# Performance work log

Measured on AMD Instinct MI355X. Metric: run time of the kernel, lower is better.

Reference implementation:

```python
import jax, jax.numpy as jnp
import numpy as np

N, M, K, C, OUT = 200000, 50000, 16, 64, 128
EPS = 1e-5  # torch BatchNorm1d default eps


def _bn(h, gamma, beta, mean, var):
    # BatchNorm1d in eval mode (running statistics)
    return (h - mean) * jax.lax.rsqrt(var + EPS) * gamma + beta


def setup_inputs() -> dict:
    key = jax.random.key(0)
    ks = jax.random.split(key, 8)
    p = jax.random.normal(ks[0], (N, 3), jnp.float32)
    x = jax.random.normal(ks[1], (N, C), jnp.float32)
    idx = jax.random.randint(ks[2], (M,), 0, N)          # FPS-sampled center indices
    knn_idx = jax.random.randint(ks[3], (M, K), 0, N)    # KNN neighbor indices
    # channel_shrinker: Linear(3+C, C, bias=False) -> BN -> ReLU -> Linear(C, 1)
    W1 = jax.random.normal(ks[4], (3 + C, C), jnp.float32) * 0.05  # stored [in,out]
    g1 = jnp.ones((C,), jnp.float32); b1 = jnp.zeros((C,), jnp.float32)
    m1 = jnp.zeros((C,), jnp.float32); v1 = jnp.ones((C,), jnp.float32)
    W2 = jax.random.normal(ks[5], (C, 1), jnp.float32) * 0.05
    b2 = jnp.zeros((1,), jnp.float32)
    # linear2: Linear(C, OUT, bias=False) -> BN -> ReLU
    Wl = jax.random.normal(ks[6], (C, OUT), jnp.float32) * 0.05
    gl = jnp.ones((OUT,), jnp.float32); bl = jnp.zeros((OUT,), jnp.float32)
    ml = jnp.zeros((OUT,), jnp.float32); vl = jnp.ones((OUT,), jnp.float32)
    return {"p": p, "x": x, "W1": W1, "g1": g1, "b1": b1, "m1": m1, "v1": v1,
            "W2": W2, "b2": b2, "Wl": Wl, "gl": gl, "bl": bl, "ml": ml, "vl": vl,
            "idx": idx, "knn_idx": knn_idx}


def reference(p, x, W1, g1, b1, m1, v1, W2, b2, Wl, gl, bl, ml, vl, idx, knn_idx):
    # queryandgroup(use_xyz=True): relative xyz of neighbors + gathered features
    n_p = p[idx]                                   # [M,3] sampled centers
    rel = p[knn_idx] - n_p[:, None, :]             # [M,K,3]
    x_knn = jnp.concatenate([rel, x[knn_idx]], -1) # [M,K,3+C]
    # channel_shrinker
    h = jnp.maximum(_bn(x_knn @ W1, g1, b1, m1, v1), 0.0)   # [M,K,C]
    s = h @ W2 + b2                                          # [M,K,1]
    prob = jax.nn.softmax(s, axis=1)                         # softmax over neighbors
    # linear2 on ALL original points, then gather by knn_idx
    y = jnp.maximum(_bn(x @ Wl, gl, bl, ml, vl), 0.0)        # [N,OUT]
    y_knn = y[knn_idx]                                       # [M,K,OUT]
    out = jnp.sum(y_knn * prob, axis=1)                      # [M,OUT]
    return n_p, out
```

## Files before the change

### kernel.cpp

```cpp
#include <hip/hip_runtime.h>

#define EPS 1e-5f

typedef __attribute__((ext_vector_type(8))) short bf16x8;
typedef __attribute__((ext_vector_type(4))) float f32x4;

static __device__ __forceinline__ unsigned short f2bf(float f) {
  unsigned int u = __float_as_uint(f);
  u = u + 0x7FFFu + ((u >> 16) & 1u);
  return (unsigned short)(u >> 16);
}
static __device__ __forceinline__ float bf2f(unsigned short h) {
  return __uint_as_float(((unsigned int)h) << 16);
}
static __device__ __forceinline__ unsigned int pk2(float lo, float hi) {
  return (unsigned int)f2bf(lo) | ((unsigned int)f2bf(hi) << 16);
}

__global__ __launch_bounds__(256) void k1_mfma(
    const float* __restrict__ x, const float* __restrict__ W1,
    const float* __restrict__ Wl, const float* __restrict__ gl,
    const float* __restrict__ bl, const float* __restrict__ ml,
    const float* __restrict__ vl,
    unsigned short* __restrict__ Z, unsigned short* __restrict__ Y)
{
  __shared__ unsigned short As[64 * 64];
  __shared__ unsigned short Bs[192 * 64];
  char* Ab = reinterpret_cast<char*>(As);
  char* Bb = reinterpret_cast<char*>(Bs);

  const int t = threadIdx.x;
  const long row0 = (long)blockIdx.x * 64;

  {
    int k = t >> 2, c0 = (t & 3) * 16;
    const float4* w4 = reinterpret_cast<const float4*>(W1 + (size_t)(3 + k) * 64 + c0);
#pragma unroll
    for (int i = 0; i < 4; ++i) {
      float4 w = w4[i];
#pragma unroll
      for (int j = 0; j < 4; ++j) {
        int c = c0 + i * 4 + j;
        float v = (j == 0) ? w.x : (j == 1) ? w.y : (j == 2) ? w.z : w.w;
        int byte = c * 128 + ((2 * k) ^ ((c & 7) << 4));
        *reinterpret_cast<unsigned short*>(Bb + byte) = f2bf(v);
      }
    }
  }
  {
    int k = t >> 2, c0 = (t & 3) * 32;
    const float4* w4 = reinterpret_cast<const float4*>(Wl + (size_t)k * 128 + c0);
#pragma unroll
    for (int i = 0; i < 8; ++i) {
      float4 w = w4[i];
#pragma unroll
      for (int j = 0; j < 4; ++j) {
        int c = 64 + c0 + i * 4 + j;
        float v = (j == 0) ? w.x : (j == 1) ? w.y : (j == 2) ? w.z : w.w;
        int byte = c * 128 + ((2 * k) ^ ((c & 7) << 4));
        *reinterpret_cast<unsigned short*>(Bb + byte) = f2bf(v);
      }
    }
  }
  {
    const float4* xg = reinterpret_cast<const float4*>(x + row0 * 64);
#pragma unroll
    for (int i = 0; i < 4; ++i) {
      int idx = t + i * 256;
      float4 v = xg[idx];
      int r = idx >> 4;
      int b0 = (idx & 15) * 8;
      int byte = r * 128 + (b0 ^ ((r & 7) << 4));
      uint2 pk = make_uint2(pk2(v.x, v.y), pk2(v.z, v.w));
      *reinterpret_cast<uint2*>(Ab + byte) = pk;
    }
  }
  __syncthreads();

  const int wid = t >> 6, lane = t & 63;
  const int roff = (wid & 1) * 32, coff = (wid >> 1) * 96;
  const int lr = lane & 15, lk = lane >> 4;

  bf16x8 af[2][2];
#pragma unroll
  for (int rt = 0; rt < 2; ++rt) {
    int r = roff + rt * 16 + lr;
#pragma unroll
    for (int ks = 0; ks < 2; ++ks) {
      int byte = r * 128 + ((ks * 64 + lk * 16) ^ ((r & 7) << 4));
      af[rt][ks] = *reinterpret_cast<const bf16x8*>(Ab + byte);
    }
  }

#pragma unroll
  for (int ct = 0; ct < 6; ++ct) {
    int c = coff + ct * 16 + lr;
    int byte0 = c * 128 + ((lk * 16) ^ ((c & 7) << 4));
    int byte1 = c * 128 + ((64 + lk * 16) ^ ((c & 7) << 4));
    bf16x8 bf0 = *reinterpret_cast<const bf16x8*>(Bb + byte0);
    bf16x8 bf1 = *reinterpret_cast<const bf16x8*>(Bb + byte1);

    float sc = 1.f, sh = 0.f;
    if (c >= 64) {
      int oc = c - 64;
      sc = gl[oc] * rsqrtf(vl[oc] + EPS);
      sh = bl[oc] - ml[oc] * sc;
    }
#pragma unroll
    for (int rt = 0; rt < 2; ++rt) {
      f32x4 acc = {0.f, 0.f, 0.f, 0.f};
      acc = __builtin_amdgcn_mfma_f32_16x16x32_bf16(af[rt][0], bf0, acc, 0, 0, 0);
      acc = __builtin_amdgcn_mfma_f32_16x16x32_bf16(af[rt][1], bf1, acc, 0, 0, 0);
      long grow = row0 + roff + rt * 16 + lk * 4;
      if (c < 64) {
#pragma unroll
        for (int q = 0; q < 4; ++q)
          Z[(grow + q) * 64 + c] = f2bf(acc[q]);
      } else {
        int oc = c - 64;
#pragma unroll
        for (int q = 0; q < 4; ++q) {
          float yv = fmaxf(fmaf(acc[q], sc, sh), 0.f);
          Y[(grow + q) * 128 + oc] = f2bf(yv);
        }
      }
    }
  }
}

__global__ __launch_bounds__(256) void k2_gather(
    const float* __restrict__ p, const unsigned short* __restrict__ Z,
    const unsigned short* __restrict__ Y, const float* __restrict__ W1,
    const float* __restrict__ g1, const float* __restrict__ b1,
    const float* __restrict__ m1, const float* __restrict__ v1,
    const float* __restrict__ W2, const int* __restrict__ idx,
    const int* __restrict__ knn, float* __restrict__ out_np,
    float* __restrict__ out_feat, int M)
{
  int gtid = blockIdx.x * 256 + threadIdx.x;
  int wid = gtid >> 6;
  int lane = threadIdx.x & 63;
  if (wid >= M) return;
  int m = __builtin_amdgcn_readfirstlane(wid);

  float a1 = g1[lane] * rsqrtf(v1[lane] + EPS);
  float c1 = b1[lane] - m1[lane] * a1;
  float w2 = W2[lane];
  float w10 = W1[lane];
  float w11 = W1[64 + lane];
  float w12 = W1[128 + lane];

  int ic = idx[m];
  float cx = p[ic * 3 + 0];
  float cy = p[ic * 3 + 1];
  float cz = p[ic * 3 + 2];
  if (lane < 3) {
    float v = (lane == 0) ? cx : ((lane == 1) ? cy : cz);
    out_np[(size_t)m * 3 + lane] = v;
  }

  float s[16];
  int jj[16];
#pragma unroll
  for (int k = 0; k < 16; ++k) {
    int j = knn[m * 16 + k];
    jj[k] = j;
    float rx = p[j * 3 + 0] - cx;
    float ry = p[j * 3 + 1] - cy;
    float rz = p[j * 3 + 2] - cz;
    float tv = bf2f(Z[(size_t)j * 64 + lane]);
    tv = fmaf(rx, w10, tv);
    tv = fmaf(ry, w11, tv);
    tv = fmaf(rz, w12, tv);
    float h = fmaxf(fmaf(tv, a1, c1), 0.f);
    float part = h * w2;
#pragma unroll
    for (int off = 32; off > 0; off >>= 1)
      part += __shfl_xor(part, off, 64);
    s[k] = part;
  }

  float mx = s[0];
#pragma unroll
  for (int k = 1; k < 16; ++k) mx = fmaxf(mx, s[k]);
  float sum = 0.f;
#pragma unroll
  for (int k = 0; k < 16; ++k) { s[k] = __expf(s[k] - mx); sum += s[k]; }
  float inv = 1.f / sum;

  float acc0 = 0.f, acc1 = 0.f;
#pragma unroll
  for (int k = 0; k < 16; ++k) {
    const unsigned short* yr = Y + (size_t)jj[k] * 128;
    unsigned int u = *reinterpret_cast<const unsigned int*>(yr + 2 * lane);
    acc0 = fmaf(s[k], bf2f((unsigned short)(u & 0xFFFFu)), acc0);
    acc1 = fmaf(s[k], bf2f((unsigned short)(u >> 16)), acc1);
  }
  float* orow = out_feat + (size_t)m * 128;
  *reinterpret_cast<float2*>(orow + 2 * lane) =
      make_float2(acc0 * inv, acc1 * inv);
}

extern "C" void kernel_launch(void* const* d_in, const int* in_sizes, int n_in,
                              void* d_out, int out_size, void* d_ws, size_t ws_size,
                              hipStream_t stream) {
  const float* p  = (const float*)d_in[0];
  const float* x  = (const float*)d_in[1];
  const float* W1 = (const float*)d_in[2];
  const float* g1 = (const float*)d_in[3];
  const float* b1 = (const float*)d_in[4];
  const float* m1 = (const float*)d_in[5];
  const float* v1 = (const float*)d_in[6];
  const float* W2 = (const float*)d_in[7];
  const float* Wl = (const float*)d_in[9];
  const float* gl = (const float*)d_in[10];
  const float* bl = (const float*)d_in[11];
  const float* ml = (const float*)d_in[12];
  const float* vl = (const float*)d_in[13];
  const int* idx  = (const int*)d_in[14];
  const int* knn  = (const int*)d_in[15];

  const int N = in_sizes[1] / 64;
  const int M = in_sizes[14];

  unsigned short* Z = (unsigned short*)d_ws;
  unsigned short* Y = Z + (size_t)N * 64;
  float* out_np   = (float*)d_out;
  float* out_feat = out_np + (size_t)M * 3;

  k1_mfma<<<dim3(N / 64), dim3(256), 0, stream>>>(
      x, W1, Wl, gl, bl, ml, vl, Z, Y);
  k2_gather<<<dim3(((size_t)M * 64 + 255) / 256), dim3(256), 0, stream>>>(
      p, Z, Y, W1, g1, b1, m1, v1, W2, idx, knn, out_np, out_feat, M);
}
```

Baseline: 219.7 us.

## Vectorize k1 output stores via swapped MFMA operands and batch k2 shuffle reductions

```diff
diff --git a/kernel.cpp b/kernel.cpp
--- a/kernel.cpp
+++ b/kernel.cpp
@@ -71,8 +71,8 @@
       int r = idx >> 4;
       int b0 = (idx & 15) * 8;
       int byte = r * 128 + (b0 ^ ((r & 7) << 4));
-      uint2 pk = make_uint2(pk2(v.x, v.y), pk2(v.z, v.w));
-      *reinterpret_cast<uint2*>(Ab + byte) = pk;
+      uint2 pkv = make_uint2(pk2(v.x, v.y), pk2(v.z, v.w));
+      *reinterpret_cast<uint2*>(Ab + byte) = pkv;
     }
   }
   __syncthreads();
@@ -94,38 +94,54 @@
 
 #pragma unroll
   for (int ct = 0; ct < 6; ++ct) {
-    int c = coff + ct * 16 + lr;
-    int byte0 = c * 128 + ((lk * 16) ^ ((c & 7) << 4));
-    int byte1 = c * 128 + ((64 + lk * 16) ^ ((c & 7) << 4));
+    int c0t = coff + ct * 16;
+    int cread = c0t + lr;
+    int byte0 = cread * 128 + ((lk * 16) ^ ((cread & 7) << 4));
+    int byte1 = cread * 128 + ((64 + lk * 16) ^ ((cread & 7) << 4));
     bf16x8 bf0 = *reinterpret_cast<const bf16x8*>(Bb + byte0);
     bf16x8 bf1 = *reinterpret_cast<const bf16x8*>(Bb + byte1);
 
-    float sc = 1.f, sh = 0.f;
-    if (c >= 64) {
-      int oc = c - 64;
-      sc = gl[oc] * rsqrtf(vl[oc] + EPS);
-      sh = bl[oc] - ml[oc] * sc;
+    float sc0 = 1.f, sc1 = 1.f, sc2 = 1.f, sc3 = 1.f;
+    float sh0 = 0.f, sh1 = 0.f, sh2 = 0.f, sh3 = 0.f;
+    if (c0t >= 64) {
+      int oc = c0t - 64 + lk * 4;
+      float4 g4 = *reinterpret_cast<const float4*>(gl + oc);
+      float4 v4 = *reinterpret_cast<const float4*>(vl + oc);
+      float4 b4 = *reinterpret_cast<const float4*>(bl + oc);
+      float4 m4 = *reinterpret_cast<const float4*>(ml + oc);
+      sc0 = g4.x * rsqrtf(v4.x + EPS); sh0 = b4.x - m4.x * sc0;
+      sc1 = g4.y * rsqrtf(v4.y + EPS); sh1 = b4.y - m4.y * sc1;
+      sc2 = g4.z * rsqrtf(v4.z + EPS); sh2 = b4.z - m4.z * sc2;
+      sc3 = g4.w * rsqrtf(v4.w + EPS); sh3 = b4.w - m4.w * sc3;
     }
 #pragma unroll
     for (int rt = 0; rt < 2; ++rt) {
       f32x4 acc = {0.f, 0.f, 0.f, 0.f};
-      acc = __builtin_amdgcn_mfma_f32_16x16x32_bf16(af[rt][0], bf0, acc, 0, 0, 0);
-      acc = __builtin_amdgcn_mfma_f32_16x16x32_bf16(af[rt][1], bf1, acc, 0, 0, 0);
-      long grow = row0 + roff + rt * 16 + lk * 4;
-      if (c < 64) {
-#pragma unroll
-        for (int q = 0; q < 4; ++q)
-          Z[(grow + q) * 64 + c] = f2bf(acc[q]);
+      acc = __builtin_amdgcn_mfma_f32_16x16x32_bf16(bf0, af[rt][0], acc, 0, 0, 0);
+      acc = __builtin_amdgcn_mfma_f32_16x16x32_bf16(bf1, af[rt][1], acc, 0, 0, 0);
+      long n = row0 + roff + rt * 16 + lr;
+      if (c0t < 64) {
+        int cb = c0t + lk * 4;
+        *reinterpret_cast<ushort4*>(Z + n * 64 + cb) =
+            make_ushort4(f2bf(acc[0]), f2bf(acc[1]), f2bf(acc[2]), f2bf(acc[3]));
       } else {
-        int oc = c - 64;
-#pragma unroll
-        for (int q = 0; q < 4; ++q) {
-          float yv = fmaxf(fmaf(acc[q], sc, sh), 0.f);
-          Y[(grow + q) * 128 + oc] = f2bf(yv);
-        }
+        int cb = c0t - 64 + lk * 4;
+        float y0 = fmaxf(fmaf(acc[0], sc0, sh0), 0.f);
+        float y1 = fmaxf(fmaf(acc[1], sc1, sh1), 0.f);
+        float y2 = fmaxf(fmaf(acc[2], sc2, sh2), 0.f);
+        float y3 = fmaxf(fmaf(acc[3], sc3, sh3), 0.f);
+        *reinterpret_cast<ushort4*>(Y + n * 128 + cb) =
+            make_ushort4(f2bf(y0), f2bf(y1), f2bf(y2), f2bf(y3));
       }
     }
   }
+}
+
+static __device__ __forceinline__ float comb(float a, float b, int off, int lane) {
+  bool hi = (lane & off) != 0;
+  float send = hi ? a : b;
+  float t = __shfl_xor(send, off, 64);
+  return (hi ? b : a) + t;
 }
 
 __global__ __launch_bounds__(256) void k2_gather(
@@ -159,7 +175,7 @@
     out_np[(size_t)m * 3 + lane] = v;
   }
 
-  float s[16];
+  float part[16];
   int jj[16];
 #pragma unroll
   for (int k = 0; k < 16; ++k) {
@@ -173,28 +189,46 @@
     tv = fmaf(ry, w11, tv);
     tv = fmaf(rz, w12, tv);
     float h = fmaxf(fmaf(tv, a1, c1), 0.f);
-    float part = h * w2;
-#pragma unroll
-    for (int off = 32; off > 0; off >>= 1)
-      part += __shfl_xor(part, off, 64);
-    s[k] = part;
-  }
-
-  float mx = s[0];
-#pragma unroll
-  for (int k = 1; k < 16; ++k) mx = fmaxf(mx, s[k]);
-  float sum = 0.f;
-#pragma unroll
-  for (int k = 0; k < 16; ++k) { s[k] = __expf(s[k] - mx); sum += s[k]; }
-  float inv = 1.f / sum;
+    part[k] = h * w2;
+  }
+
+  float u[8];
+#pragma unroll
+  for (int i = 0; i < 8; ++i) u[i] = comb(part[2 * i], part[2 * i + 1], 32, lane);
+  float v4[4];
+#pragma unroll
+  for (int i = 0; i < 4; ++i) v4[i] = comb(u[2 * i], u[2 * i + 1], 16, lane);
+  float w4[2];
+#pragma unroll
+  for (int i = 0; i < 2; ++i) w4[i] = comb(v4[2 * i], v4[2 * i + 1], 8, lane);
+  float s1 = comb(w4[0], w4[1], 4, lane);
+  s1 += __shfl_xor(s1, 1, 64);
+  s1 += __shfl_xor(s1, 2, 64);
+
+  float mx = s1;
+  mx = fmaxf(mx, __shfl_xor(mx, 4, 64));
+  mx = fmaxf(mx, __shfl_xor(mx, 8, 64));
+  mx = fmaxf(mx, __shfl_xor(mx, 16, 64));
+  mx = fmaxf(mx, __shfl_xor(mx, 32, 64));
+  float e = __expf(s1 - mx);
+
+  float pk[16];
+  float S = 0.f;
+#pragma unroll
+  for (int k = 0; k < 16; ++k) {
+    int g = ((k & 1) << 3) | ((k & 2) << 1) | ((k & 4) >> 1) | ((k & 8) >> 3);
+    pk[k] = __shfl(e, g * 4, 64);
+    S += pk[k];
+  }
+  float inv = 1.f / S;
 
   float acc0 = 0.f, acc1 = 0.f;
 #pragma unroll
   for (int k = 0; k < 16; ++k) {
     const unsigned short* yr = Y + (size_t)jj[k] * 128;
-    unsigned int u = *reinterpret_cast<const unsigned int*>(yr + 2 * lane);
-    acc0 = fmaf(s[k], bf2f((unsigned short)(u & 0xFFFFu)), acc0);
-    acc1 = fmaf(s[k], bf2f((unsigned short)(u >> 16)), acc1);
+    unsigned int uu = *reinterpret_cast<const unsigned int*>(yr + 2 * lane);
+    acc0 = fmaf(pk[k], bf2f((unsigned short)(uu & 0xFFFFu)), acc0);
+    acc1 = fmaf(pk[k], bf2f((unsigned short)(uu >> 16)), acc1);
   }
   float* orow = out_feat + (size_t)m * 128;
   *reinterpret_cast<float2*>(orow + 2 * lane) =
```

After: 226.0 us. 2.9% more time.
